# Kernel tuning notes

Measured on AMD Instinct MI355X. Metric: run time of the kernel, lower is better.

Reference implementation:

```python
import jax, jax.numpy as jnp
import numpy as np

QUERY_DIM = 512
CAAN_DIM = 512
HID = 30

def setup_inputs() -> dict:
    key = jax.random.key(0)
    ks = jax.random.split(key, 9)
    def lin(kk, out_d, in_d):
        lim = 1.0 / np.sqrt(in_d)
        return jax.random.uniform(kk, (out_d, in_d), jnp.float32, -lim, lim)
    R = jax.random.normal(ks[0], (8, 2048, QUERY_DIM), jnp.float32)
    return {
        "R": R,
        "Wq": lin(ks[1], CAAN_DIM, QUERY_DIM), "bq": jnp.zeros((CAAN_DIM,), jnp.float32),
        "Wk": lin(ks[2], CAAN_DIM, QUERY_DIM), "bk": jnp.zeros((CAAN_DIM,), jnp.float32),
        "Wv": lin(ks[3], CAAN_DIM, QUERY_DIM), "bv": jnp.zeros((CAAN_DIM,), jnp.float32),
        "W1": lin(ks[4], HID, CAAN_DIM), "b1": jax.random.uniform(ks[5], (HID,), jnp.float32, -1/np.sqrt(CAAN_DIM), 1/np.sqrt(CAAN_DIM)),
        "W2": lin(ks[6], 1, HID), "b2": jax.random.uniform(ks[7], (1,), jnp.float32, -1/np.sqrt(HID), 1/np.sqrt(HID)),
    }

def reference(R, Wq, bq, Wk, bk, Wv, bv, W1, b1, W2, b2):
    # Projections: [b, n, d]
    Q = jnp.einsum('bnq,dq->bnd', R, Wq) + bq
    K = jnp.einsum('bnq,dq->bnd', R, Wk) + bk
    V = jnp.einsum('bnq,dq->bnd', R, Wv) + bv
    dk = K.shape[-1]
    # Full score matrix, naive exp-normalize (no max subtraction) as in original
    gamma = jnp.einsum('bnd,bmd->bnm', Q, K) / jnp.sqrt(jnp.float32(dk))
    e = jnp.exp(gamma)
    saat = e / jnp.sum(e, axis=2, keepdims=True)  # [b, n, n]
    a = jnp.einsum('bnm,bmd->bnd', saat, V)       # [b, n, d]
    # fc head: CAAN_dim -> 30 -> 1, squeeze last dim
    h = jnp.einsum('bnd,hd->bnh', a, W1) + b1
    winner_score = (jnp.einsum('bnh,oh->bno', h, W2) + b2)[..., 0]
    return winner_score
```

## Files before the change

### kernel.cpp

```cpp
#include <hip/hip_runtime.h>
#include <math.h>

#define BATCH 8
#define SEQ 2048
#define DIM 512
#define MTOT (BATCH*SEQ)
#define HID 30

typedef short bf16x8 __attribute__((ext_vector_type(8)));
typedef float f32x4 __attribute__((ext_vector_type(4)));

__device__ __forceinline__ unsigned short f2bf(float f) {
  unsigned int u = __float_as_uint(f);
  unsigned int r = (u + 0x7FFFu + ((u >> 16) & 1u)) >> 16;
  return (unsigned short)r;
}
__device__ __forceinline__ float bf2f(unsigned short u) {
  return __uint_as_float((unsigned int)u << 16);
}

__device__ __forceinline__ void gload_lds16(const void* g, void* l) {
  __builtin_amdgcn_global_load_lds((const __attribute__((address_space(1))) void*)g,
                                   (__attribute__((address_space(3))) void*)l, 16, 0, 0);
}

__device__ __forceinline__ void gemm256_core(const unsigned short* __restrict__ gA,
                                             const unsigned short* __restrict__ gB,
                                             char* smem, f32x4 (&acc)[8][4]) {
  const int t = threadIdx.x;
  const int lane = t & 63;
  const int w = t >> 6;
  const int wr = w >> 2, wc = w & 3;
  const int lr = lane & 15, kc = lane >> 4;
  const int srow = t >> 3;
  const int ss = (t & 7) ^ (srow & 7);
  const unsigned short* gsrc = (ss < 4 ? gA : gB) + (size_t)srow * DIM + (ss & 3) * 8;
  const uint32_t dbase = (uint32_t)(t & 448) * 16;

  auto stage = [&](int buf, int kt) {
#pragma unroll
    for (int q = 0; q < 4; ++q)
      gload_lds16(gsrc + (size_t)(q * 64) * DIM + kt * 32,
                  smem + buf * 32768 + q * 8192 + dbase);
  };

  stage(0, 0); stage(1, 1); stage(2, 2);
  asm volatile("s_waitcnt vmcnt(8)" ::: "memory");
  __builtin_amdgcn_s_barrier();
  asm volatile("" ::: "memory");

#pragma unroll
  for (int kt = 0; kt < 16; ++kt) {
    stage((kt + 3) & 3, (kt + 3 < 16) ? (kt + 3) : 15);
    const char* Ab = smem + (kt & 3) * 32768;
    bf16x8 bfr[4], af[4];
#pragma unroll
    for (int j = 0; j < 4; ++j) {
      int r = wc * 64 + j * 16 + lr;
      bfr[j] = *(const bf16x8*)(Ab + r * 128 + (((4 + kc) ^ (r & 7)) << 4));
    }
#pragma unroll
    for (int i = 0; i < 4; ++i) {
      int r = wr * 128 + i * 16 + lr;
      af[i] = *(const bf16x8*)(Ab + r * 128 + ((kc ^ (r & 7)) << 4));
    }
    __builtin_amdgcn_s_setprio(1);
#pragma unroll
    for (int i = 0; i < 4; ++i)
#pragma unroll
      for (int j = 0; j < 4; ++j)
        acc[i][j] = __builtin_amdgcn_mfma_f32_16x16x32_bf16(af[i], bfr[j], acc[i][j], 0, 0, 0);
    __builtin_amdgcn_s_setprio(0);
#pragma unroll
    for (int i = 0; i < 4; ++i) {
      int r = wr * 128 + (i + 4) * 16 + lr;
      af[i] = *(const bf16x8*)(Ab + r * 128 + ((kc ^ (r & 7)) << 4));
    }
    __builtin_amdgcn_s_setprio(1);
#pragma unroll
    for (int i = 0; i < 4; ++i)
#pragma unroll
      for (int j = 0; j < 4; ++j)
        acc[i + 4][j] = __builtin_amdgcn_mfma_f32_16x16x32_bf16(af[i], bfr[j], acc[i + 4][j], 0, 0, 0);
    __builtin_amdgcn_s_setprio(0);
    asm volatile("s_waitcnt vmcnt(8)" ::: "memory");
    __builtin_amdgcn_s_barrier();
    asm volatile("" ::: "memory");
  }
}

__global__ __launch_bounds__(256) void k_setup(
    const float* __restrict__ R, const float* __restrict__ Wq, const float* __restrict__ Wk,
    const float* __restrict__ Wv, const float* __restrict__ bq, const float* __restrict__ bv,
    const float* __restrict__ W1, const float* __restrict__ b1,
    const float* __restrict__ W2, const float* __restrict__ b2,
    unsigned short* __restrict__ Gt, unsigned short* __restrict__ Rb16,
    float* __restrict__ u, float* __restrict__ wv2, float* __restrict__ consts) {
  __shared__ __align__(16) float As[16][68];
  __shared__ __align__(16) float Bs[16][68];
  __shared__ float w12s[512];
  __shared__ float red[256];
  const int bid = blockIdx.x;
  const int t = threadIdx.x;

  if (bid >= 66) {
    size_t base = ((size_t)(bid - 66) * 256 + t) * 8;
    float4 r0 = *(const float4*)&R[base];
    float4 r1 = *(const float4*)&R[base + 4];
    ushort4 lo, hi;
    lo.x = f2bf(r0.x); lo.y = f2bf(r0.y); lo.z = f2bf(r0.z); lo.w = f2bf(r0.w);
    hi.x = f2bf(r1.x); hi.y = f2bf(r1.y); hi.z = f2bf(r1.z); hi.w = f2bf(r1.w);
    *(ushort4*)&Rb16[base] = lo;
    *(ushort4*)&Rb16[base + 4] = hi;
    return;
  }
  if (bid == 64) {
    for (int q = t; q < DIM; q += 256) {
      float s = 0.f;
      for (int j = 0; j < HID; ++j) s = fmaf(W2[j], W1[(size_t)j * DIM + q], s);
      w12s[q] = s;
    }
    __syncthreads();
    for (int q = t; q < DIM; q += 256) {
      float s = 0.f;
      for (int d = 0; d < DIM; ++d) s = fmaf(Wv[(size_t)d * DIM + q], w12s[d], s);
      wv2[q] = s;
    }
    red[t] = bv[t] * w12s[t] + bv[t + 256] * w12s[t + 256];
    __syncthreads();
    for (int o = 128; o > 0; o >>= 1) {
      if (t < o) red[t] += red[t + o];
      __syncthreads();
    }
    if (t == 0) {
      consts[0] = red[0];
      float s = b2[0];
      for (int j = 0; j < HID; ++j) s = fmaf(W2[j], b1[j], s);
      consts[1] = s;
    }
    return;
  }
  if (bid == 65) {
    for (int q = t; q < DIM; q += 256) {
      float s = 0.f;
      for (int d = 0; d < DIM; ++d) s = fmaf(bq[d], Wk[(size_t)d * DIM + q], s);
      u[q] = s;
    }
    return;
  }
  int tm = t & 15, tn = t >> 4;
  int q1b = (bid & 7) * 64, q2b = (bid >> 3) * 64;
  int lk = t >> 4, lc = (t & 15) * 4;
  float acc[4][4] = {};
  for (int kb = 0; kb < DIM; kb += 16) {
    *(float4*)&As[lk][lc] = *(const float4*)&Wq[(size_t)(kb + lk) * DIM + q1b + lc];
    *(float4*)&Bs[lk][lc] = *(const float4*)&Wk[(size_t)(kb + lk) * DIM + q2b + lc];
    __syncthreads();
#pragma unroll
    for (int k = 0; k < 16; ++k) {
      float4 av = *(float4*)&As[k][tm * 4];
      float4 bv4 = *(float4*)&Bs[k][tn * 4];
      float a[4] = {av.x, av.y, av.z, av.w};
      float b[4] = {bv4.x, bv4.y, bv4.z, bv4.w};
#pragma unroll
      for (int i = 0; i < 4; ++i)
#pragma unroll
        for (int j = 0; j < 4; ++j) acc[i][j] = fmaf(a[i], b[j], acc[i][j]);
    }
    __syncthreads();
  }
#pragma unroll
  for (int i = 0; i < 4; ++i)
#pragma unroll
    for (int j = 0; j < 4; ++j)
      Gt[(size_t)(q2b + tn * 4 + j) * DIM + (q1b + tm * 4 + i)] = f2bf(acc[i][j]);
}

__global__ __launch_bounds__(256) void k_vw(const unsigned short* __restrict__ Rb16,
                                            const float* __restrict__ wv2,
                                            const float* __restrict__ consts,
                                            float* __restrict__ vw) {
  __shared__ float wv2s[512];
  int t = threadIdx.x;
  wv2s[t] = wv2[t];
  wv2s[t + 256] = wv2[t + 256];
  __syncthreads();
  int n = blockIdx.x * 4 + (t >> 6);
  int lane = t & 63;
  bf16x8 rv = *(const bf16x8*)&Rb16[(size_t)n * DIM + lane * 8];
  float s = 0.f;
#pragma unroll
  for (int e = 0; e < 8; ++e) s = fmaf(bf2f((unsigned short)rv[e]), wv2s[lane * 8 + e], s);
#pragma unroll
  for (int o = 32; o > 0; o >>= 1) s += __shfl_xor(s, o);
  if (lane == 0) vw[n] = s + consts[0];
}

__global__ __launch_bounds__(512, 2) void k_projT(const unsigned short* __restrict__ Rb16,
                                                  const unsigned short* __restrict__ Gt,
                                                  const float* __restrict__ u,
                                                  unsigned short* __restrict__ Tb16) {
  __shared__ __align__(16) char smem[131072];
  __shared__ float u_lds[256];
  int t = threadIdx.x;
  size_t rowb = (size_t)blockIdx.x * 256;
  int colb = blockIdx.y * 256;
  if (t < 256) u_lds[t] = u[colb + t];
  f32x4 acc[8][4] = {};
  gemm256_core(Rb16 + rowb * DIM, Gt + (size_t)colb * DIM, smem, acc);
  int lane = t & 63, w = t >> 6, wr = w >> 2, wc = w & 3;
  int lr = lane & 15, kq = lane >> 4;
#pragma unroll
  for (int i = 0; i < 8; ++i)
#pragma unroll
    for (int j = 0; j < 4; ++j)
#pragma unroll
      for (int r = 0; r < 4; ++r) {
        int row = wr * 128 + i * 16 + kq * 4 + r;
        int col = wc * 64 + j * 16 + lr;
        Tb16[(rowb + row) * DIM + colb + col] = f2bf(acc[i][j][r] + u_lds[col]);
      }
}

__global__ __launch_bounds__(512, 2) void k_qk(const unsigned short* __restrict__ Tb16,
                                               const unsigned short* __restrict__ Rb16,
                                               const float* __restrict__ vw,
                                               float* __restrict__ part_s1,
                                               float* __restrict__ part_den) {
  __shared__ __align__(16) char smem[131072];
  __shared__ float vw_lds[256];
  __shared__ float red_s1[4][256], red_den[4][256];
  int t = threadIdx.x;
  int orig = blockIdx.x;
  int wgid = (orig & 7) * 64 + (orig >> 3);
  int b = wgid >> 6;
  int nb = ((wgid >> 3) & 7) * 256;
  int mb = (wgid & 7) * 256;
  if (t < 256) vw_lds[t] = vw[b * SEQ + mb + t];
  f32x4 acc[8][4] = {};
  gemm256_core(Tb16 + ((size_t)b * SEQ + nb) * DIM,
               Rb16 + ((size_t)b * SEQ + mb) * DIM, smem, acc);
  int lane = t & 63, w = t >> 6, wr = w >> 2, wc = w & 3;
  int lr = lane & 15, kq = lane >> 4;
  const float rs = 0.044194173824159216f;
  float vwl[4];
#pragma unroll
  for (int j = 0; j < 4; ++j) vwl[j] = vw_lds[wc * 64 + j * 16 + lr];
#pragma unroll
  for (int i = 0; i < 8; ++i) {
#pragma unroll
    for (int r = 0; r < 4; ++r) {
      float sa = 0.f, sd = 0.f;
#pragma unroll
      for (int j = 0; j < 4; ++j) {
        float e = __expf(acc[i][j][r] * rs);
        sa = fmaf(e, vwl[j], sa);
        sd += e;
      }
#pragma unroll
      for (int m = 1; m < 16; m <<= 1) { sa += __shfl_xor(sa, m); sd += __shfl_xor(sd, m); }
      if (lr == 0) {
        int rl = wr * 128 + i * 16 + kq * 4 + r;
        red_s1[wc][rl] = sa;
        red_den[wc][rl] = sd;
      }
    }
  }
  __syncthreads();
  if (t < 256) {
    size_t o = ((size_t)b * 8 + (mb >> 8)) * SEQ + nb + t;
    part_s1[o] = red_s1[0][t] + red_s1[1][t] + red_s1[2][t] + red_s1[3][t];
    part_den[o] = red_den[0][t] + red_den[1][t] + red_den[2][t] + red_den[3][t];
  }
}

__global__ void k_final(const float* __restrict__ part_s1, const float* __restrict__ part_den,
                        const float* __restrict__ consts, float* __restrict__ out) {
  int n = blockIdx.x * 256 + threadIdx.x;
  int b = n >> 11, nn = n & 2047;
  float s1 = 0.f, dn = 0.f;
#pragma unroll
  for (int i = 0; i < 8; ++i) {
    size_t o = ((size_t)b * 8 + i) * SEQ + nn;
    s1 += part_s1[o];
    dn += part_den[o];
  }
  out[n] = s1 / dn + consts[1];
}

extern "C" void kernel_launch(void* const* d_in, const int* in_sizes, int n_in,
                              void* d_out, int out_size, void* d_ws, size_t ws_size,
                              hipStream_t stream) {
  const float* R  = (const float*)d_in[0];
  const float* Wq = (const float*)d_in[1];
  const float* bq = (const float*)d_in[2];
  const float* Wk = (const float*)d_in[3];
  const float* bk = (const float*)d_in[4];
  const float* Wv = (const float*)d_in[5];
  const float* bv = (const float*)d_in[6];
  const float* W1 = (const float*)d_in[7];
  const float* b1 = (const float*)d_in[8];
  const float* W2 = (const float*)d_in[9];
  const float* b2 = (const float*)d_in[10];
  (void)bk;
  float* out = (float*)d_out;

  char* p = (char*)d_ws;
  unsigned short* Rb16 = (unsigned short*)p; p += (size_t)MTOT * DIM * 2;
  unsigned short* Tb16 = (unsigned short*)p; p += (size_t)MTOT * DIM * 2;
  unsigned short* Gt   = (unsigned short*)p; p += (size_t)DIM * DIM * 2;
  float* part_s1  = (float*)p; p += (size_t)BATCH * 8 * SEQ * 4;
  float* part_den = (float*)p; p += (size_t)BATCH * 8 * SEQ * 4;
  float* u      = (float*)p; p += DIM * 4;
  float* wv2    = (float*)p; p += DIM * 4;
  float* vw     = (float*)p; p += MTOT * 4;
  float* consts = (float*)p; p += 16;

  hipLaunchKernelGGL(k_setup, dim3(66 + MTOT * DIM / (256 * 8)), dim3(256), 0, stream,
                     R, Wq, Wk, Wv, bq, bv, W1, b1, W2, b2, Gt, Rb16, u, wv2, consts);
  hipLaunchKernelGGL(k_vw, dim3(MTOT / 4), dim3(256), 0, stream, Rb16, wv2, consts, vw);
  hipLaunchKernelGGL(k_projT, dim3(MTOT / 256, DIM / 256), dim3(512), 0, stream,
                     Rb16, Gt, u, Tb16);
  hipLaunchKernelGGL(k_qk, dim3(512), dim3(512), 0, stream, Tb16, Rb16, vw, part_s1, part_den);
  hipLaunchKernelGGL(k_final, dim3(MTOT / 256), dim3(256), 0, stream,
                     part_s1, part_den, consts, out);
}
```

Baseline: 114.1 us.

## Split weight setup across blocks and fuse R conversion with vw dot product

The setup kernel no longer converts R to bf16. A new k_weights kernel spreads the u and wv2 matrix-vector products over 64 blocks instead of one block each, and register-prefetches the Wq/Wk tiles in the small Gt GEMM. R conversion and the vw dot product are fused into one k_conv kernel that reads fp32 R once and skips re-reading Rb16. This removes the serial single-block tail and one pass over Rb16. The trade-off is that vw is now computed from fp32 rather than bf16 values.

```diff
diff --git a/kernel.cpp b/kernel.cpp
--- a/kernel.cpp
+++ b/kernel.cpp
@@ -14,9 +14,6 @@
   unsigned int u = __float_as_uint(f);
   unsigned int r = (u + 0x7FFFu + ((u >> 16) & 1u)) >> 16;
   return (unsigned short)r;
-}
-__device__ __forceinline__ float bf2f(unsigned short u) {
-  return __uint_as_float((unsigned int)u << 16);
 }
 
 __device__ __forceinline__ void gload_lds16(const void* g, void* l) {
@@ -89,44 +86,98 @@
   }
 }
 
-__global__ __launch_bounds__(256) void k_setup(
-    const float* __restrict__ R, const float* __restrict__ Wq, const float* __restrict__ Wk,
-    const float* __restrict__ Wv, const float* __restrict__ bq, const float* __restrict__ bv,
+__global__ __launch_bounds__(256) void k_weights(
+    const float* __restrict__ Wq, const float* __restrict__ Wk, const float* __restrict__ Wv,
+    const float* __restrict__ bq, const float* __restrict__ bv,
     const float* __restrict__ W1, const float* __restrict__ b1,
     const float* __restrict__ W2, const float* __restrict__ b2,
-    unsigned short* __restrict__ Gt, unsigned short* __restrict__ Rb16,
-    float* __restrict__ u, float* __restrict__ wv2, float* __restrict__ consts) {
+    unsigned short* __restrict__ Gt, float* __restrict__ u,
+    float* __restrict__ wv2, float* __restrict__ consts) {
   __shared__ __align__(16) float As[16][68];
   __shared__ __align__(16) float Bs[16][68];
-  __shared__ float w12s[512];
-  __shared__ float red[256];
+  __shared__ float vecs[512];
+  __shared__ float red2[16][17];
   const int bid = blockIdx.x;
   const int t = threadIdx.x;
 
-  if (bid >= 66) {
-    size_t base = ((size_t)(bid - 66) * 256 + t) * 8;
-    float4 r0 = *(const float4*)&R[base];
-    float4 r1 = *(const float4*)&R[base + 4];
-    ushort4 lo, hi;
-    lo.x = f2bf(r0.x); lo.y = f2bf(r0.y); lo.z = f2bf(r0.z); lo.w = f2bf(r0.w);
-    hi.x = f2bf(r1.x); hi.y = f2bf(r1.y); hi.z = f2bf(r1.z); hi.w = f2bf(r1.w);
-    *(ushort4*)&Rb16[base] = lo;
-    *(ushort4*)&Rb16[base + 4] = hi;
+  if (bid < 64) {
+    int tm = t & 15, tn = t >> 4;
+    int q1b = (bid & 7) * 64, q2b = (bid >> 3) * 64;
+    int lk = t >> 4, lc = (t & 15) * 4;
+    float acc[4][4] = {};
+    float4 ra = *(const float4*)&Wq[(size_t)lk * DIM + q1b + lc];
+    float4 rb = *(const float4*)&Wk[(size_t)lk * DIM + q2b + lc];
+    for (int kb = 0; kb < DIM; kb += 16) {
+      *(float4*)&As[lk][lc] = ra;
+      *(float4*)&Bs[lk][lc] = rb;
+      __syncthreads();
+      if (kb + 16 < DIM) {
+        ra = *(const float4*)&Wq[(size_t)(kb + 16 + lk) * DIM + q1b + lc];
+        rb = *(const float4*)&Wk[(size_t)(kb + 16 + lk) * DIM + q2b + lc];
+      }
+#pragma unroll
+      for (int k = 0; k < 16; ++k) {
+        float4 av = *(float4*)&As[k][tm * 4];
+        float4 bv4 = *(float4*)&Bs[k][tn * 4];
+        float a[4] = {av.x, av.y, av.z, av.w};
+        float b[4] = {bv4.x, bv4.y, bv4.z, bv4.w};
+#pragma unroll
+        for (int i = 0; i < 4; ++i)
+#pragma unroll
+          for (int j = 0; j < 4; ++j) acc[i][j] = fmaf(a[i], b[j], acc[i][j]);
+      }
+      __syncthreads();
+    }
+#pragma unroll
+    for (int i = 0; i < 4; ++i)
+#pragma unroll
+      for (int j = 0; j < 4; ++j)
+        Gt[(size_t)(q2b + tn * 4 + j) * DIM + (q1b + tm * 4 + i)] = f2bf(acc[i][j]);
     return;
   }
-  if (bid == 64) {
-    for (int q = t; q < DIM; q += 256) {
+
+  if (bid < 128) {
+    bool isU = bid < 96;
+    int qb = (bid - (isU ? 64 : 96)) * 16;
+    if (isU) {
+      vecs[t] = bq[t];
+      vecs[t + 256] = bq[t + 256];
+    } else {
+      for (int d = t; d < DIM; d += 256) {
+        float s = 0.f;
+        for (int j = 0; j < HID; ++j) s = fmaf(W2[j], W1[(size_t)j * DIM + d], s);
+        vecs[d] = s;
+      }
+    }
+    __syncthreads();
+    const float* M = isU ? Wk : Wv;
+    int ql = t & 15, ds = t >> 4;
+    float s = 0.f;
+#pragma unroll 8
+    for (int i = 0; i < 32; ++i) {
+      int d = ds * 32 + i;
+      s = fmaf(vecs[d], M[(size_t)d * DIM + qb + ql], s);
+    }
+    red2[ds][ql] = s;
+    __syncthreads();
+    if (t < 16) {
+      float r = 0.f;
+#pragma unroll
+      for (int k = 0; k < 16; ++k) r += red2[k][t];
+      (isU ? u : wv2)[qb + t] = r;
+    }
+    return;
+  }
+
+  {
+    for (int d = t; d < DIM; d += 256) {
       float s = 0.f;
-      for (int j = 0; j < HID; ++j) s = fmaf(W2[j], W1[(size_t)j * DIM + q], s);
-      w12s[q] = s;
+      for (int j = 0; j < HID; ++j) s = fmaf(W2[j], W1[(size_t)j * DIM + d], s);
+      vecs[d] = s;
     }
     __syncthreads();
-    for (int q = t; q < DIM; q += 256) {
-      float s = 0.f;
-      for (int d = 0; d < DIM; ++d) s = fmaf(Wv[(size_t)d * DIM + q], w12s[d], s);
-      wv2[q] = s;
-    }
-    red[t] = bv[t] * w12s[t] + bv[t + 256] * w12s[t + 256];
+    float* red = (float*)red2;
+    red[t] = bv[t] * vecs[t] + bv[t + 256] * vecs[t + 256];
     __syncthreads();
     for (int o = 128; o > 0; o >>= 1) {
       if (t < o) red[t] += red[t + o];
@@ -138,62 +189,31 @@
       for (int j = 0; j < HID; ++j) s = fmaf(W2[j], b1[j], s);
       consts[1] = s;
     }
-    return;
-  }
-  if (bid == 65) {
-    for (int q = t; q < DIM; q += 256) {
-      float s = 0.f;
-      for (int d = 0; d < DIM; ++d) s = fmaf(bq[d], Wk[(size_t)d * DIM + q], s);
-      u[q] = s;
-    }
-    return;
-  }
-  int tm = t & 15, tn = t >> 4;
-  int q1b = (bid & 7) * 64, q2b = (bid >> 3) * 64;
-  int lk = t >> 4, lc = (t & 15) * 4;
-  float acc[4][4] = {};
-  for (int kb = 0; kb < DIM; kb += 16) {
-    *(float4*)&As[lk][lc] = *(const float4*)&Wq[(size_t)(kb + lk) * DIM + q1b + lc];
-    *(float4*)&Bs[lk][lc] = *(const float4*)&Wk[(size_t)(kb + lk) * DIM + q2b + lc];
-    __syncthreads();
-#pragma unroll
-    for (int k = 0; k < 16; ++k) {
-      float4 av = *(float4*)&As[k][tm * 4];
-      float4 bv4 = *(float4*)&Bs[k][tn * 4];
-      float a[4] = {av.x, av.y, av.z, av.w};
-      float b[4] = {bv4.x, bv4.y, bv4.z, bv4.w};
-#pragma unroll
-      for (int i = 0; i < 4; ++i)
-#pragma unroll
-        for (int j = 0; j < 4; ++j) acc[i][j] = fmaf(a[i], b[j], acc[i][j]);
-    }
-    __syncthreads();
-  }
-#pragma unroll
-  for (int i = 0; i < 4; ++i)
-#pragma unroll
-    for (int j = 0; j < 4; ++j)
-      Gt[(size_t)(q2b + tn * 4 + j) * DIM + (q1b + tm * 4 + i)] = f2bf(acc[i][j]);
-}
-
-__global__ __launch_bounds__(256) void k_vw(const unsigned short* __restrict__ Rb16,
-                                            const float* __restrict__ wv2,
-                                            const float* __restrict__ consts,
-                                            float* __restrict__ vw) {
-  __shared__ float wv2s[512];
-  int t = threadIdx.x;
-  wv2s[t] = wv2[t];
-  wv2s[t + 256] = wv2[t + 256];
-  __syncthreads();
-  int n = blockIdx.x * 4 + (t >> 6);
-  int lane = t & 63;
-  bf16x8 rv = *(const bf16x8*)&Rb16[(size_t)n * DIM + lane * 8];
-  float s = 0.f;
-#pragma unroll
-  for (int e = 0; e < 8; ++e) s = fmaf(bf2f((unsigned short)rv[e]), wv2s[lane * 8 + e], s);
-#pragma unroll
-  for (int o = 32; o > 0; o >>= 1) s += __shfl_xor(s, o);
-  if (lane == 0) vw[n] = s + consts[0];
+  }
+}
+
+__global__ __launch_bounds__(256) void k_conv(const float* __restrict__ R,
+                                              const float* __restrict__ wv2,
+                                              const float* __restrict__ consts,
+                                              unsigned short* __restrict__ Rb16,
+                                              float* __restrict__ vw) {
+  int wave = threadIdx.x >> 6, lane = threadIdx.x & 63;
+  size_t n = (size_t)blockIdx.x * 4 + wave;
+  const float* p = &R[n * DIM + lane * 8];
+  float4 r0 = *(const float4*)p;
+  float4 r1 = *(const float4*)(p + 4);
+  ushort4 lo, hi;
+  lo.x = f2bf(r0.x); lo.y = f2bf(r0.y); lo.z = f2bf(r0.z); lo.w = f2bf(r0.w);
+  hi.x = f2bf(r1.x); hi.y = f2bf(r1.y); hi.z = f2bf(r1.z); hi.w = f2bf(r1.w);
+  *(ushort4*)&Rb16[n * DIM + lane * 8] = lo;
+  *(ushort4*)&Rb16[n * DIM + lane * 8 + 4] = hi;
+  float4 v0 = *(const float4*)&wv2[lane * 8];
+  float4 v1 = *(const float4*)&wv2[lane * 8 + 4];
+  float sv = r0.x * v0.x + r0.y * v0.y + r0.z * v0.z + r0.w * v0.w +
+             r1.x * v1.x + r1.y * v1.y + r1.z * v1.z + r1.w * v1.w;
+#pragma unroll
+  for (int o = 32; o > 0; o >>= 1) sv += __shfl_xor(sv, o);
+  if (lane == 0) vw[n] = sv + consts[0];
 }
 
 __global__ __launch_bounds__(512, 2) void k_projT(const unsigned short* __restrict__ Rb16,
@@ -316,9 +336,9 @@
   float* vw     = (float*)p; p += MTOT * 4;
   float* consts = (float*)p; p += 16;
 
-  hipLaunchKernelGGL(k_setup, dim3(66 + MTOT * DIM / (256 * 8)), dim3(256), 0, stream,
-                     R, Wq, Wk, Wv, bq, bv, W1, b1, W2, b2, Gt, Rb16, u, wv2, consts);
-  hipLaunchKernelGGL(k_vw, dim3(MTOT / 4), dim3(256), 0, stream, Rb16, wv2, consts, vw);
+  hipLaunchKernelGGL(k_weights, dim3(129), dim3(256), 0, stream,
+                     Wq, Wk, Wv, bq, bv, W1, b1, W2, b2, Gt, u, wv2, consts);
+  hipLaunchKernelGGL(k_conv, dim3(MTOT / 4), dim3(256), 0, stream, R, wv2, consts, Rb16, vw);
   hipLaunchKernelGGL(k_projT, dim3(MTOT / 256, DIM / 256), dim3(512), 0, stream,
                      Rb16, Gt, u, Tb16);
   hipLaunchKernelGGL(k_qk, dim3(512), dim3(512), 0, stream, Tb16, Rb16, vw, part_s1, part_den);
```

Result: faster. 101.2 us (-11.3%).
